# Performance work log

Measured on AMD Instinct MI355X. Metric: run time of the kernel, lower is better.

The kernel has to match this reference:

```python
import jax, jax.numpy as jnp
import numpy as np

N = 200000      # nodes
SDIM = 256      # scalar feature dim
VDIM = 64       # vector feature channels (each a 3-vector)
B = 512         # number of graphs (segments)
EPS = 1e-06


def setup_inputs() -> dict:
    key = jax.random.key(0)
    k1, k2, k3 = jax.random.split(key, 3)
    s = jax.random.normal(k1, (N, SDIM), dtype=jnp.float32)
    v = jax.random.normal(k2, (N, VDIM, 3), dtype=jnp.float32)
    batch = jnp.sort(jax.random.randint(k3, (N,), 0, B, dtype=jnp.int64))
    weight = jnp.ones((SDIM,), dtype=jnp.float32)
    bias = jnp.zeros((SDIM,), dtype=jnp.float32)
    return {"s": s, "v": v, "batch": batch, "weight": weight, "bias": bias}


def reference(s, v, batch, weight, bias):
    # per-segment counts, clamped to 1 (scatter_mean semantics)
    cnt = jax.ops.segment_sum(jnp.ones((s.shape[0],), s.dtype), batch, num_segments=B)
    cnt = jnp.maximum(cnt, 1.0)[:, None]                       # [B, 1]

    # scalar branch: segment mean/var normalize + affine
    smean = jax.ops.segment_sum(s, batch, num_segments=B) / cnt   # [B, SDIM]
    sc = s - smean[batch]                                          # [N, SDIM]
    var = jax.ops.segment_sum(sc * sc, batch, num_segments=B) / cnt
    prec = 1.0 / jnp.sqrt(jnp.maximum(var, EPS))                  # [B, SDIM]
    sout = sc * prec[batch] * weight + bias                        # [N, SDIM]

    # vector branch: divide by segment-mean squared norm per channel
    vsq = jnp.sum(v * v, axis=-1, keepdims=True)                  # [N, VDIM, 1]
    vmean = jax.ops.segment_sum(vsq, batch, num_segments=B) / cnt[:, :, None]
    vmean = jnp.maximum(vmean, EPS)                                # [B, VDIM, 1]
    vout = v / vmean[batch]                                        # [N, VDIM, 3]

    return (sout, vout)
```

## Files before the change

kernel.cpp:

```cpp
#include <hip/hip_runtime.h>

#define SDIM   256
#define VDIM   64
#define VFLAT  192
#define SG4    64
#define VG4    48
#define BSEG   512
#define NLANES 16
#define EPS    1e-6f

typedef float nfloat4 __attribute__((ext_vector_type(4)));

__device__ inline void acc4(float4& a, const float4& b) {
    a.x += b.x; a.y += b.y; a.z += b.z; a.w += b.w;
}
__device__ inline void fma4(float4& a, const float4& x) {
    a.x += x.x * x.x; a.y += x.y * x.y; a.z += x.z * x.z; a.w += x.w * x.w;
}
__device__ inline float4 ntload4(const float* p) {
    nfloat4 r = __builtin_nontemporal_load((const nfloat4*)p);
    return make_float4(r.x, r.y, r.z, r.w);
}
__device__ inline void ntstore4(float* p, float4 v) {
    nfloat4 r = {v.x, v.y, v.z, v.w};
    __builtin_nontemporal_store(r, (nfloat4*)p);
}

__global__ __launch_bounds__(1024) void segnorm_kernel(
    const float* __restrict__ s,
    const float* __restrict__ v,
    const int*   __restrict__ batch,
    const float* __restrict__ weight,
    const float* __restrict__ bias,
    float* __restrict__ sout,
    float* __restrict__ vout,
    int n_nodes)
{
    const int b   = blockIdx.x;
    const int tid = threadIdx.x;
    const int g   = tid & 63;
    const int nid = tid >> 6;

    __shared__ int    seg_bounds[2];
    __shared__ float4 red0[NLANES][SG4];
    __shared__ float4 red1[NLANES][SG4];
    __shared__ float4 lds_a[SG4];
    __shared__ float4 lds_b[SG4];
    __shared__ float  lds_vpf[VFLAT];
    __shared__ float  lds_vinv[VDIM];

    if (tid < 2) {
        const int key = b + tid;
        int lo = 0, hi = n_nodes;
        while (lo < hi) {
            int mid = (lo + hi) >> 1;
            if (batch[mid] < key) lo = mid + 1; else hi = mid;
        }
        seg_bounds[tid] = lo;
    }
    __syncthreads();
    const int lo = seg_bounds[0];
    const int hi = seg_bounds[1];
    const float cnt     = fmaxf((float)(hi - lo), 1.0f);
    const float inv_cnt = 1.0f / cnt;

    const float* srow = s + 4 * g;
    const float* vrow = v + 4 * g;

    float4 ssum4 = {0.f, 0.f, 0.f, 0.f};
    float4 ssq4  = {0.f, 0.f, 0.f, 0.f};
    float4 vp4   = {0.f, 0.f, 0.f, 0.f};
    int n = lo + nid;
    for (; n + NLANES < hi; n += 2 * NLANES) {
        const int n1 = n + NLANES;
        float4 x0 = *(const float4*)(srow + (size_t)n  * SDIM);
        float4 x1 = *(const float4*)(srow + (size_t)n1 * SDIM);
        float4 y0, y1;
        if (g < VG4) {
            y0 = *(const float4*)(vrow + (size_t)n  * VFLAT);
            y1 = *(const float4*)(vrow + (size_t)n1 * VFLAT);
        }
        acc4(ssum4, x0); fma4(ssq4, x0);
        acc4(ssum4, x1); fma4(ssq4, x1);
        if (g < VG4) { fma4(vp4, y0); fma4(vp4, y1); }
    }
    for (; n < hi; n += NLANES) {
        float4 x = *(const float4*)(srow + (size_t)n * SDIM);
        acc4(ssum4, x); fma4(ssq4, x);
        if (g < VG4) {
            float4 y = *(const float4*)(vrow + (size_t)n * VFLAT);
            fma4(vp4, y);
        }
    }

    red0[nid][g] = ssum4;
    red1[nid][g] = ssq4;
    __syncthreads();
    for (int st = NLANES / 2; st >= 1; st >>= 1) {
        if (nid < st) {
            acc4(red0[nid][g], red0[nid + st][g]);
            acc4(red1[nid][g], red1[nid + st][g]);
        }
        __syncthreads();
    }
    if (nid == 0) {
        float4 sum = red0[0][g], sq = red1[0][g];
        float4 w4 = *(const float4*)(weight + 4 * g);
        float4 b4 = *(const float4*)(bias + 4 * g);
        float4 a_, b_;
        {
            float m = sum.x * inv_cnt, var = sq.x * inv_cnt - m * m;
            float p = 1.0f / sqrtf(fmaxf(var, EPS));
            a_.x = p * w4.x; b_.x = b4.x - m * a_.x;
        }
        {
            float m = sum.y * inv_cnt, var = sq.y * inv_cnt - m * m;
            float p = 1.0f / sqrtf(fmaxf(var, EPS));
            a_.y = p * w4.y; b_.y = b4.y - m * a_.y;
        }
        {
            float m = sum.z * inv_cnt, var = sq.z * inv_cnt - m * m;
            float p = 1.0f / sqrtf(fmaxf(var, EPS));
            a_.z = p * w4.z; b_.z = b4.z - m * a_.z;
        }
        {
            float m = sum.w * inv_cnt, var = sq.w * inv_cnt - m * m;
            float p = 1.0f / sqrtf(fmaxf(var, EPS));
            a_.w = p * w4.w; b_.w = b4.w - m * a_.w;
        }
        lds_a[g] = a_;
        lds_b[g] = b_;
    }
    __syncthreads();

    red0[nid][g] = (g < VG4) ? vp4 : make_float4(0.f, 0.f, 0.f, 0.f);
    __syncthreads();
    for (int st = NLANES / 2; st >= 1; st >>= 1) {
        if (nid < st) acc4(red0[nid][g], red0[nid + st][g]);
        __syncthreads();
    }
    if (nid == 0 && g < VG4) {
        float4 t = red0[0][g];
        lds_vpf[4 * g + 0] = t.x;
        lds_vpf[4 * g + 1] = t.y;
        lds_vpf[4 * g + 2] = t.z;
        lds_vpf[4 * g + 3] = t.w;
    }
    __syncthreads();
    if (tid < VDIM) {
        float vm = (lds_vpf[3 * tid] + lds_vpf[3 * tid + 1] + lds_vpf[3 * tid + 2]) * inv_cnt;
        lds_vinv[tid] = 1.0f / fmaxf(vm, EPS);
    }
    __syncthreads();

    const float4 a4 = lds_a[g];
    const float4 b4 = lds_b[g];
    float4 vi4 = {0.f, 0.f, 0.f, 0.f};
    if (g < VG4) {
        vi4.x = lds_vinv[(4 * g + 0) / 3];
        vi4.y = lds_vinv[(4 * g + 1) / 3];
        vi4.z = lds_vinv[(4 * g + 2) / 3];
        vi4.w = lds_vinv[(4 * g + 3) / 3];
    }

    float* so = sout + 4 * g;
    float* vo = vout + 4 * g;

    n = lo + nid;
    for (; n + NLANES < hi; n += 2 * NLANES) {
        const int n1 = n + NLANES;
        float4 x0 = ntload4(srow + (size_t)n  * SDIM);
        float4 x1 = ntload4(srow + (size_t)n1 * SDIM);
        float4 y0, y1;
        if (g < VG4) {
            y0 = ntload4(vrow + (size_t)n  * VFLAT);
            y1 = ntload4(vrow + (size_t)n1 * VFLAT);
        }
        float4 o0, o1;
        o0.x = x0.x * a4.x + b4.x; o0.y = x0.y * a4.y + b4.y;
        o0.z = x0.z * a4.z + b4.z; o0.w = x0.w * a4.w + b4.w;
        o1.x = x1.x * a4.x + b4.x; o1.y = x1.y * a4.y + b4.y;
        o1.z = x1.z * a4.z + b4.z; o1.w = x1.w * a4.w + b4.w;
        ntstore4(so + (size_t)n  * SDIM, o0);
        ntstore4(so + (size_t)n1 * SDIM, o1);
        if (g < VG4) {
            float4 u0, u1;
            u0.x = y0.x * vi4.x; u0.y = y0.y * vi4.y;
            u0.z = y0.z * vi4.z; u0.w = y0.w * vi4.w;
            u1.x = y1.x * vi4.x; u1.y = y1.y * vi4.y;
            u1.z = y1.z * vi4.z; u1.w = y1.w * vi4.w;
            ntstore4(vo + (size_t)n  * VFLAT, u0);
            ntstore4(vo + (size_t)n1 * VFLAT, u1);
        }
    }
    for (; n < hi; n += NLANES) {
        float4 x = ntload4(srow + (size_t)n * SDIM);
        float4 o;
        o.x = x.x * a4.x + b4.x; o.y = x.y * a4.y + b4.y;
        o.z = x.z * a4.z + b4.z; o.w = x.w * a4.w + b4.w;
        ntstore4(so + (size_t)n * SDIM, o);
        if (g < VG4) {
            float4 y = ntload4(vrow + (size_t)n * VFLAT);
            float4 u;
            u.x = y.x * vi4.x; u.y = y.y * vi4.y;
            u.z = y.z * vi4.z; u.w = y.w * vi4.w;
            ntstore4(vo + (size_t)n * VFLAT, u);
        }
    }
}

extern "C" void kernel_launch(void* const* d_in, const int* in_sizes, int n_in,
                              void* d_out, int out_size, void* d_ws, size_t ws_size,
                              hipStream_t stream)
{
    const float* s      = (const float*)d_in[0];
    const float* v      = (const float*)d_in[1];
    const int*   batch  = (const int*)  d_in[2];
    const float* weight = (const float*)d_in[3];
    const float* bias   = (const float*)d_in[4];

    const int n_nodes = in_sizes[2];

    float* sout = (float*)d_out;
    float* vout = sout + (size_t)n_nodes * SDIM;

    segnorm_kernel<<<dim3(BSEG), dim3(1024), 0, stream>>>(
        s, v, batch, weight, bias, sout, vout, n_nodes);
}
```

Measured before the change: 171.7 us.

## Split into stats kernel and flat node-parallel normalize kernel via workspace

Result: slower. 191.6 us (+11.6%).

```diff
diff --git a/kernel.cpp b/kernel.cpp
--- a/kernel.cpp
+++ b/kernel.cpp
@@ -9,6 +9,9 @@
 #define NLANES 16
 #define EPS    1e-6f
 
+#define NBLK   2048
+#define NTHR   256
+
 typedef float nfloat4 __attribute__((ext_vector_type(4)));
 
 __device__ inline void acc4(float4& a, const float4& b) {
@@ -26,14 +29,15 @@
     __builtin_nontemporal_store(r, (nfloat4*)p);
 }
 
-__global__ __launch_bounds__(1024) void segnorm_kernel(
+__global__ __launch_bounds__(1024) void stats_kernel(
     const float* __restrict__ s,
     const float* __restrict__ v,
     const int*   __restrict__ batch,
     const float* __restrict__ weight,
     const float* __restrict__ bias,
-    float* __restrict__ sout,
-    float* __restrict__ vout,
+    float4* __restrict__ wsA,
+    float4* __restrict__ wsB,
+    float*  __restrict__ wsV,
     int n_nodes)
 {
     const int b   = blockIdx.x;
@@ -44,10 +48,7 @@
     __shared__ int    seg_bounds[2];
     __shared__ float4 red0[NLANES][SG4];
     __shared__ float4 red1[NLANES][SG4];
-    __shared__ float4 lds_a[SG4];
-    __shared__ float4 lds_b[SG4];
     __shared__ float  lds_vpf[VFLAT];
-    __shared__ float  lds_vinv[VDIM];
 
     if (tid < 2) {
         const int key = b + tid;
@@ -71,19 +72,26 @@
     float4 ssq4  = {0.f, 0.f, 0.f, 0.f};
     float4 vp4   = {0.f, 0.f, 0.f, 0.f};
     int n = lo + nid;
-    for (; n + NLANES < hi; n += 2 * NLANES) {
-        const int n1 = n + NLANES;
+    for (; n + 3 * NLANES < hi; n += 4 * NLANES) {
+        const int n1 = n + NLANES, n2 = n + 2 * NLANES, n3 = n + 3 * NLANES;
         float4 x0 = *(const float4*)(srow + (size_t)n  * SDIM);
         float4 x1 = *(const float4*)(srow + (size_t)n1 * SDIM);
-        float4 y0, y1;
+        float4 x2 = *(const float4*)(srow + (size_t)n2 * SDIM);
+        float4 x3 = *(const float4*)(srow + (size_t)n3 * SDIM);
+        float4 y0, y1, y2, y3;
         if (g < VG4) {
             y0 = *(const float4*)(vrow + (size_t)n  * VFLAT);
             y1 = *(const float4*)(vrow + (size_t)n1 * VFLAT);
+            y2 = *(const float4*)(vrow + (size_t)n2 * VFLAT);
+            y3 = *(const float4*)(vrow + (size_t)n3 * VFLAT);
         }
         acc4(ssum4, x0); fma4(ssq4, x0);
         acc4(ssum4, x1); fma4(ssq4, x1);
-        if (g < VG4) { fma4(vp4, y0); fma4(vp4, y1); }
-    }
+        acc4(ssum4, x2); fma4(ssq4, x2);
+        acc4(ssum4, x3); fma4(ssq4, x3);
+        if (g < VG4) { fma4(vp4, y0); fma4(vp4, y1); fma4(vp4, y2); fma4(vp4, y3); }
+    }
+#pragma clang loop unroll(disable)
     for (; n < hi; n += NLANES) {
         float4 x = *(const float4*)(srow + (size_t)n * SDIM);
         acc4(ssum4, x); fma4(ssq4, x);
@@ -128,8 +136,8 @@
             float p = 1.0f / sqrtf(fmaxf(var, EPS));
             a_.w = p * w4.w; b_.w = b4.w - m * a_.w;
         }
-        lds_a[g] = a_;
-        lds_b[g] = b_;
+        wsA[b * SG4 + g] = a_;
+        wsB[b * SG4 + g] = b_;
     }
     __syncthreads();
 
@@ -149,58 +157,58 @@
     __syncthreads();
     if (tid < VDIM) {
         float vm = (lds_vpf[3 * tid] + lds_vpf[3 * tid + 1] + lds_vpf[3 * tid + 2]) * inv_cnt;
-        lds_vinv[tid] = 1.0f / fmaxf(vm, EPS);
-    }
-    __syncthreads();
-
-    const float4 a4 = lds_a[g];
-    const float4 b4 = lds_b[g];
-    float4 vi4 = {0.f, 0.f, 0.f, 0.f};
-    if (g < VG4) {
-        vi4.x = lds_vinv[(4 * g + 0) / 3];
-        vi4.y = lds_vinv[(4 * g + 1) / 3];
-        vi4.z = lds_vinv[(4 * g + 2) / 3];
-        vi4.w = lds_vinv[(4 * g + 3) / 3];
-    }
-
+        wsV[b * VDIM + tid] = 1.0f / fmaxf(vm, EPS);
+    }
+}
+
+__global__ __launch_bounds__(NTHR) void norm_kernel(
+    const float* __restrict__ s,
+    const float* __restrict__ v,
+    const int*   __restrict__ batch,
+    const float4* __restrict__ wsA,
+    const float4* __restrict__ wsB,
+    const float*  __restrict__ wsV,
+    float* __restrict__ sout,
+    float* __restrict__ vout,
+    int n_nodes, int nodes_per_blk)
+{
+    const int tid = threadIdx.x;
+    const int g   = tid & 63;
+    const int nid = tid >> 6;
+
+    const int base = blockIdx.x * nodes_per_blk;
+    const int end  = min(base + nodes_per_blk, n_nodes);
+
+    const float* srow = s + 4 * g;
+    const float* vrow = v + 4 * g;
     float* so = sout + 4 * g;
     float* vo = vout + 4 * g;
 
-    n = lo + nid;
-    for (; n + NLANES < hi; n += 2 * NLANES) {
-        const int n1 = n + NLANES;
-        float4 x0 = ntload4(srow + (size_t)n  * SDIM);
-        float4 x1 = ntload4(srow + (size_t)n1 * SDIM);
-        float4 y0, y1;
-        if (g < VG4) {
-            y0 = ntload4(vrow + (size_t)n  * VFLAT);
-            y1 = ntload4(vrow + (size_t)n1 * VFLAT);
-        }
-        float4 o0, o1;
-        o0.x = x0.x * a4.x + b4.x; o0.y = x0.y * a4.y + b4.y;
-        o0.z = x0.z * a4.z + b4.z; o0.w = x0.w * a4.w + b4.w;
-        o1.x = x1.x * a4.x + b4.x; o1.y = x1.y * a4.y + b4.y;
-        o1.z = x1.z * a4.z + b4.z; o1.w = x1.w * a4.w + b4.w;
-        ntstore4(so + (size_t)n  * SDIM, o0);
-        ntstore4(so + (size_t)n1 * SDIM, o1);
-        if (g < VG4) {
-            float4 u0, u1;
-            u0.x = y0.x * vi4.x; u0.y = y0.y * vi4.y;
-            u0.z = y0.z * vi4.z; u0.w = y0.w * vi4.w;
-            u1.x = y1.x * vi4.x; u1.y = y1.y * vi4.y;
-            u1.z = y1.z * vi4.z; u1.w = y1.w * vi4.w;
-            ntstore4(vo + (size_t)n  * VFLAT, u0);
-            ntstore4(vo + (size_t)n1 * VFLAT, u1);
-        }
-    }
-    for (; n < hi; n += NLANES) {
+    int cur_seg = -1;
+    float4 a4 = {0,0,0,0}, b4 = {0,0,0,0}, vi4 = {0,0,0,0};
+
+    for (int n = base + nid; n < end; n += 4) {
+        const int seg = batch[n];
+        if (seg != cur_seg) {
+            cur_seg = seg;
+            a4 = wsA[seg * SG4 + g];
+            b4 = wsB[seg * SG4 + g];
+            if (g < VG4) {
+                const float* vv = wsV + seg * VDIM;
+                vi4.x = vv[(4 * g + 0) / 3];
+                vi4.y = vv[(4 * g + 1) / 3];
+                vi4.z = vv[(4 * g + 2) / 3];
+                vi4.w = vv[(4 * g + 3) / 3];
+            }
+        }
         float4 x = ntload4(srow + (size_t)n * SDIM);
+        float4 y;
+        if (g < VG4) y = ntload4(vrow + (size_t)n * VFLAT);
         float4 o;
         o.x = x.x * a4.x + b4.x; o.y = x.y * a4.y + b4.y;
         o.z = x.z * a4.z + b4.z; o.w = x.w * a4.w + b4.w;
         ntstore4(so + (size_t)n * SDIM, o);
         if (g < VG4) {
-            float4 y = ntload4(vrow + (size_t)n * VFLAT);
             float4 u;
             u.x = y.x * vi4.x; u.y = y.y * vi4.y;
             u.z = y.z * vi4.z; u.w = y.w * vi4.w;
@@ -224,6 +232,14 @@
     float* sout = (float*)d_out;
     float* vout = sout + (size_t)n_nodes * SDIM;
 
-    segnorm_kernel<<<dim3(BSEG), dim3(1024), 0, stream>>>(
-        s, v, batch, weight, bias, sout, vout, n_nodes);
-}
+    float4* wsA = (float4*)d_ws;
+    float4* wsB = wsA + (size_t)BSEG * SG4;
+    float*  wsV = (float*)(wsB + (size_t)BSEG * SG4);
+
+    stats_kernel<<<dim3(BSEG), dim3(1024), 0, stream>>>(
+        s, v, batch, weight, bias, wsA, wsB, wsV, n_nodes);
+
+    const int npb = (n_nodes + NBLK - 1) / NBLK;
+    norm_kernel<<<dim3(NBLK), dim3(NTHR), 0, stream>>>(
+        s, v, batch, wsA, wsB, wsV, sout, vout, n_nodes, npb);
+}
```
